# Performance work log

Measured on AMD Instinct MI355X. Metric: run time of the kernel, lower is better.

## Reference

```python
import jax, jax.numpy as jnp
import numpy as np

N = 200000          # active input voxels
GRID = 96           # voxel grid extent
_OFFS = np.array([[dx, dy, dz] for dx in (-1, 0, 1) for dy in (-1, 0, 1) for dz in (-1, 0, 1)], dtype=np.int64)  # 27 kernel offsets


def _build_kmap(cin, cout, stride):
    """Build gather/scatter kernel maps for a 3x3x3 sparse conv.
    For each offset k and each output j, find input i with coord_in[i] == coord_out[j]*stride + off[k].
    Misses scatter to sentinel row n_out (dropped) and gather row 0 (value ignored)."""
    B = int(max(cin.max(), cout.max() * stride + 1)) + 3
    key_in = (cin[:, 0].astype(np.int64) * B + cin[:, 1]) * B + cin[:, 2]
    order = np.argsort(key_in).astype(np.int32)
    sk = key_in[order]
    n_out = cout.shape[0]
    g = np.zeros((27, n_out), np.int32)
    s = np.full((27, n_out), n_out, np.int32)
    ar = np.arange(n_out, dtype=np.int32)
    co = cout.astype(np.int64)
    for k in range(27):
        q = co * stride + _OFFS[k]
        valid = (q >= 0).all(axis=1)
        qk = (q[:, 0] * B + q[:, 1]) * B + q[:, 2]
        pos = np.clip(np.searchsorted(sk, qk), 0, sk.shape[0] - 1)
        found = valid & (sk[pos] == qk)
        g[k] = np.where(found, order[pos], 0)
        s[k] = np.where(found, ar, n_out)
    return jnp.asarray(g), jnp.asarray(s)


def setup_inputs() -> dict:
    rng = np.random.RandomState(0)
    raw = rng.randint(0, GRID, size=(3 * N, 3))
    coords = np.unique(raw, axis=0)[:N]          # [N,3] unique voxel coords
    c1 = coords
    c2 = np.unique(c1 // 2, axis=0)              # stride-2 output coords
    g1, s1 = _build_kmap(c1, c1, 1)              # submanifold conv1
    g2, s2 = _build_kmap(c1, c2, 2)              # strided conv2
    g3, s3 = _build_kmap(c2, c2, 1)              # submanifold conv3
    key = jax.random.key(0)
    k1, k2, k3, k4 = jax.random.split(key, 4)
    feats = jax.random.normal(k1, (N, 4), jnp.float32)
    W1 = jax.random.normal(k2, (27, 4, 32), jnp.float32) * (1.0 / np.sqrt(27 * 4))
    W2 = jax.random.normal(k3, (27, 32, 32), jnp.float32) * (1.0 / np.sqrt(27 * 32))
    W3 = jax.random.normal(k4, (27, 32, 2), jnp.float32) * (1.0 / np.sqrt(27 * 32))
    return {"feats": feats, "W1": W1, "W2": W2, "W3": W3,
            "g1": g1, "s1": s1, "g2": g2, "s2": s2, "g3": g3, "s3": s3}


def _sparse_conv(feats, W, gidx, sidx):
    n_out = sidx.shape[1]
    c_out = W.shape[-1]
    gathered = feats[gidx]                              # [27, M, Cin] irregular gather
    contrib = jnp.einsum('kmc,kcd->kmd', gathered, W)   # per-offset GEMM
    out = jnp.zeros((n_out + 1, c_out), feats.dtype)    # +1 sentinel row for misses
    out = out.at[sidx.reshape(-1)].add(contrib.reshape(-1, c_out))  # scatter-add
    return out[:n_out]


def reference(feats, W1, W2, W3, g1, s1, g2, s2, g3, s3):
    x = _sparse_conv(feats, W1, g1, s1)
    x = _sparse_conv(x, W2, g2, s2)
    x = _sparse_conv(x, W3, g3, s3)
    return x
```

## Files before the change

### kernel.cpp

```cpp
#include <hip/hip_runtime.h>

#define CDIV(a,b) (((a)+(b)-1)/(b))

typedef __attribute__((ext_vector_type(8)))  short short8v;
typedef __attribute__((ext_vector_type(4)))  short short4v;
typedef __attribute__((ext_vector_type(16))) float f32x16;

__device__ inline unsigned short f2bf(float x) {
    unsigned u = __builtin_bit_cast(unsigned, x);
    u += 0x7fffu + ((u >> 16) & 1u);
    return (unsigned short)(u >> 16);
}

__global__ __launch_bounds__(256) void prep_feats_k(
    const float* __restrict__ feats, unsigned short* __restrict__ featsh,
    unsigned short* __restrict__ x1h, int N)
{
    int i = blockIdx.x * 256 + threadIdx.x;
    if (i < N) {
        float4 f = *reinterpret_cast<const float4*>(feats + (size_t)i * 4);
        ushort4 h; h.x = f2bf(f.x); h.y = f2bf(f.y); h.z = f2bf(f.z); h.w = f2bf(f.w);
        *reinterpret_cast<ushort4*>(featsh + (size_t)i * 4) = h;
    } else if (i == N) {
        *reinterpret_cast<ushort4*>(featsh + (size_t)N * 4) = make_ushort4(0, 0, 0, 0);
        #pragma unroll
        for (int t = 0; t < 8; ++t)
            *reinterpret_cast<ushort4*>(x1h + (size_t)N * 32 + t * 4) = make_ushort4(0, 0, 0, 0);
    }
}

__global__ __launch_bounds__(256) void prep_w_k(
    const float* __restrict__ W1, const float* __restrict__ W2,
    unsigned short* __restrict__ w2h, unsigned short* __restrict__ w1f)
{
    int i = blockIdx.x * 256 + threadIdx.x;
    if (i < 27 * 1024) {
        int k = i >> 10, c = (i >> 5) & 31, d = i & 31;
        w2h[k * 1024 + d * 32 + c] = f2bf(W2[i]);
    } else if (i < 27 * 1024 + 4096) {
        int idx = i - 27 * 1024;
        int m = idx >> 9, n = (idx >> 4) & 31, kk = idx & 15;
        int slot = 4 * m + (kk >> 2), c = kk & 3;
        float v = (slot < 27) ? W1[slot * 128 + c * 32 + n] : 0.f;
        w1f[m * 512 + n * 16 + kk] = f2bf(v);
    }
}

__global__ __launch_bounds__(256) void conv1_k(
    const unsigned short* __restrict__ featsh, const unsigned short* __restrict__ w1f,
    const int* __restrict__ g1, const int* __restrict__ s1,
    unsigned short* __restrict__ x1h, int N)
{
    int tid = threadIdx.x;
    int l = tid & 63, wv = tid >> 6;
    int r = l & 31, h = l >> 5;
    int rbase = blockIdx.x * 128 + wv * 32;
    int j = rbase + r;
    int jc = j < N ? j : N - 1;

    int gm[8][2];
    #pragma unroll
    for (int m = 0; m < 8; ++m)
        #pragma unroll
        for (int t = 0; t < 2; ++t) {
            int slot = 4 * m + 2 * h + t;
            int v = N;
            if (slot < 27 && j < N) {
                int s = s1[(size_t)slot * N + jc];
                int g = g1[(size_t)slot * N + jc];
                v = (s != N) ? g : N;
            }
            gm[m][t] = v;
        }

    f32x16 acc = {};
    const char* fb = (const char*)featsh;
    const char* wb = (const char*)w1f;
    #pragma unroll
    for (int m = 0; m < 8; ++m) {
        short4v lo = *(const short4v*)(fb + (size_t)gm[m][0] * 8);
        short4v hi = *(const short4v*)(fb + (size_t)gm[m][1] * 8);
        short8v a = __builtin_shufflevector(lo, hi, 0, 1, 2, 3, 4, 5, 6, 7);
        short8v b = *(const short8v*)(wb + (m * 512 + r * 16 + h * 8) * 2);
        acc = __builtin_amdgcn_mfma_f32_32x32x16_bf16(a, b, acc, 0, 0, 0);
    }
    #pragma unroll
    for (int reg = 0; reg < 16; ++reg) {
        int row = (reg & 3) + 8 * (reg >> 2) + 4 * h;
        int j2 = rbase + row;
        if (j2 < N) x1h[(size_t)j2 * 32 + r] = f2bf(acc[reg]);
    }
}

__global__ __launch_bounds__(256) void conv2_k(
    const unsigned short* __restrict__ x1h, const unsigned short* __restrict__ w2h,
    const int* __restrict__ g2, const int* __restrict__ s2,
    float* __restrict__ x2, int M, int N)
{
    int tid = threadIdx.x;
    int l = tid & 63, wv = tid >> 6;
    int r = l & 31, h = l >> 5;
    int rbase = blockIdx.x * 128 + wv * 32;
    int j = rbase + r;
    int jc = j < M ? j : M - 1;

    int gm[27];
    #pragma unroll
    for (int k = 0; k < 27; ++k) {
        int s = s2[(size_t)k * M + jc];
        int g = g2[(size_t)k * M + jc];
        gm[k] = (j < M && s != M) ? g : N;
    }

    f32x16 acc = {};
    const char* xb = (const char*)x1h;
    const char* wb = (const char*)w2h;
    #pragma unroll
    for (int k = 0; k < 27; ++k) {
        const char* xr = xb + (size_t)gm[k] * 64;
        short8v a0 = *(const short8v*)(xr + h * 16);
        short8v a1 = *(const short8v*)(xr + 32 + h * 16);
        short8v b0 = *(const short8v*)(wb + k * 2048 + r * 64 + h * 16);
        short8v b1 = *(const short8v*)(wb + k * 2048 + r * 64 + 32 + h * 16);
        acc = __builtin_amdgcn_mfma_f32_32x32x16_bf16(a0, b0, acc, 0, 0, 0);
        acc = __builtin_amdgcn_mfma_f32_32x32x16_bf16(a1, b1, acc, 0, 0, 0);
    }
    #pragma unroll
    for (int reg = 0; reg < 16; ++reg) {
        int row = (reg & 3) + 8 * (reg >> 2) + 4 * h;
        int j2 = rbase + row;
        if (j2 < M) x2[(size_t)j2 * 32 + r] = acc[reg];
    }
}

__global__ __launch_bounds__(256) void conv3_k(
    const float* __restrict__ x2, const float* __restrict__ W3,
    const int* __restrict__ g3, const int* __restrict__ s3,
    float* __restrict__ out, int M)
{
    __shared__ float w[27 * 64];
    int tid = threadIdx.x;
    for (int i = tid; i < 27 * 64; i += 256) w[i] = W3[i];
    __syncthreads();

    int q = tid & 3;
    int j = blockIdx.x * 64 + (tid >> 2);
    int jc = j < M ? j : M - 1;

    int gm[27];
    #pragma unroll
    for (int k = 0; k < 27; ++k) {
        int s = s3[(size_t)k * M + jc];
        int g = g3[(size_t)k * M + jc];
        gm[k] = (s != M) ? g : -1;
    }

    float a0 = 0.f, a1 = 0.f;
    #pragma unroll
    for (int k = 0; k < 27; ++k) {
        float m = gm[k] >= 0 ? 1.f : 0.f;
        int g = gm[k] >= 0 ? gm[k] : 0;
        const float* xr = x2 + (size_t)g * 32 + q * 8;
        float4 f0 = *(const float4*)(xr);
        float4 f1 = *(const float4*)(xr + 4);
        const float* wk = w + k * 64 + q * 16;
        float4 wA = *(const float4*)(wk);
        float4 wB = *(const float4*)(wk + 4);
        float4 wC = *(const float4*)(wk + 8);
        float4 wD = *(const float4*)(wk + 12);
        a0 += m * (f0.x * wA.x + f0.y * wA.z + f0.z * wB.x + f0.w * wB.z
                 + f1.x * wC.x + f1.y * wC.z + f1.z * wD.x + f1.w * wD.z);
        a1 += m * (f0.x * wA.y + f0.y * wA.w + f0.z * wB.y + f0.w * wB.w
                 + f1.x * wC.y + f1.y * wC.w + f1.z * wD.y + f1.w * wD.w);
    }
    a0 += __shfl_xor(a0, 1); a0 += __shfl_xor(a0, 2);
    a1 += __shfl_xor(a1, 1); a1 += __shfl_xor(a1, 2);
    if (q == 0 && j < M)
        *reinterpret_cast<float2*>(out + (size_t)j * 2) = make_float2(a0, a1);
}

extern "C" void kernel_launch(void* const* d_in, const int* in_sizes, int n_in,
                              void* d_out, int out_size, void* d_ws, size_t ws_size,
                              hipStream_t stream) {
    const float* feats = (const float*)d_in[0];
    const float* W1    = (const float*)d_in[1];
    const float* W2    = (const float*)d_in[2];
    const float* W3    = (const float*)d_in[3];
    const int*   g1    = (const int*)d_in[4];
    const int*   s1    = (const int*)d_in[5];
    const int*   g2    = (const int*)d_in[6];
    const int*   s2    = (const int*)d_in[7];
    const int*   g3    = (const int*)d_in[8];
    const int*   s3    = (const int*)d_in[9];

    int N = in_sizes[0] / 4;
    int M = in_sizes[6] / 27;

    char* wsb = (char*)d_ws;
    size_t off = 0;
    auto alloc = [&](size_t bytes) {
        char* p = wsb + off;
        off = (off + bytes + 255) & ~(size_t)255;
        return p;
    };
    unsigned short* x1h    = (unsigned short*)alloc((size_t)(N + 1) * 64);
    unsigned short* featsh = (unsigned short*)alloc((size_t)(N + 1) * 8);
    unsigned short* w2h    = (unsigned short*)alloc(27 * 1024 * 2);
    unsigned short* w1f    = (unsigned short*)alloc(8 * 512 * 2);
    float*          x2     = (float*)alloc((size_t)M * 128);
    float* out = (float*)d_out;

    prep_feats_k<<<CDIV(N + 1, 256), 256, 0, stream>>>(feats, featsh, x1h, N);
    prep_w_k<<<CDIV(27 * 1024 + 4096, 256), 256, 0, stream>>>(W1, W2, w2h, w1f);
    conv1_k<<<CDIV(N, 128), 256, 0, stream>>>(featsh, w1f, g1, s1, x1h, N);
    conv2_k<<<CDIV(M, 128), 256, 0, stream>>>(x1h, w2h, g2, s2, x2, M, N);
    conv3_k<<<CDIV(M, 64),  256, 0, stream>>>(x2, W3, g3, s3, out, M);
}
```

Before: 168.3 us.

## Merge prep kernels, store conv2 output as bf16, run conv3 on MFMA

Merges the two prep kernels into one launch. The weights are repacked into a lane-contiguous MFMA fragment layout so each lane does one coalesced 16-byte load. conv2 now writes bf16 activations instead of fp32, which halves the intermediate traffic and gather bytes for conv3. conv3 is rewritten to use 32x32x16 bf16 MFMA with zero-padded output columns and a sentinel zero row, replacing the scalar FMA path with LDS weights. This wastes most of the MFMA compute on padding columns and adds bf16 rounding on the conv2 output.

```diff
diff --git a/kernel.cpp b/kernel.cpp
--- a/kernel.cpp
+++ b/kernel.cpp
@@ -12,42 +12,59 @@
     return (unsigned short)(u >> 16);
 }
 
-__global__ __launch_bounds__(256) void prep_feats_k(
-    const float* __restrict__ feats, unsigned short* __restrict__ featsh,
-    unsigned short* __restrict__ x1h, int N)
+__global__ __launch_bounds__(256) void prep_k(
+    const float* __restrict__ feats, const float* __restrict__ W1,
+    const float* __restrict__ W2, const float* __restrict__ W3,
+    unsigned short* __restrict__ featsh, unsigned short* __restrict__ x1h,
+    unsigned short* __restrict__ x2h,
+    unsigned short* __restrict__ w1p, unsigned short* __restrict__ w2p,
+    unsigned short* __restrict__ w3p, int N, int M)
 {
     int i = blockIdx.x * 256 + threadIdx.x;
     if (i < N) {
         float4 f = *reinterpret_cast<const float4*>(feats + (size_t)i * 4);
         ushort4 h; h.x = f2bf(f.x); h.y = f2bf(f.y); h.z = f2bf(f.z); h.w = f2bf(f.w);
         *reinterpret_cast<ushort4*>(featsh + (size_t)i * 4) = h;
-    } else if (i == N) {
+        return;
+    }
+    if (i == N) {
         *reinterpret_cast<ushort4*>(featsh + (size_t)N * 4) = make_ushort4(0, 0, 0, 0);
         #pragma unroll
-        for (int t = 0; t < 8; ++t)
+        for (int t = 0; t < 8; ++t) {
             *reinterpret_cast<ushort4*>(x1h + (size_t)N * 32 + t * 4) = make_ushort4(0, 0, 0, 0);
-    }
-}
-
-__global__ __launch_bounds__(256) void prep_w_k(
-    const float* __restrict__ W1, const float* __restrict__ W2,
-    unsigned short* __restrict__ w2h, unsigned short* __restrict__ w1f)
-{
-    int i = blockIdx.x * 256 + threadIdx.x;
-    if (i < 27 * 1024) {
-        int k = i >> 10, c = (i >> 5) & 31, d = i & 31;
-        w2h[k * 1024 + d * 32 + c] = f2bf(W2[i]);
-    } else if (i < 27 * 1024 + 4096) {
-        int idx = i - 27 * 1024;
-        int m = idx >> 9, n = (idx >> 4) & 31, kk = idx & 15;
-        int slot = 4 * m + (kk >> 2), c = kk & 3;
-        float v = (slot < 27) ? W1[slot * 128 + c * 32 + n] : 0.f;
-        w1f[m * 512 + n * 16 + kk] = f2bf(v);
+            *reinterpret_cast<ushort4*>(x2h + (size_t)M * 32 + t * 4) = make_ushort4(0, 0, 0, 0);
+        }
+        return;
+    }
+    int j = i - (N + 1);
+    if (j < 4096) {
+        int m = j >> 9, t = j & 511, l = t >> 3, e = t & 7;
+        int h = l >> 5, r = l & 31;
+        int kk = h * 8 + e, slot = 4 * m + (kk >> 2), c = kk & 3;
+        float v = (slot < 27) ? W1[slot * 128 + c * 32 + r] : 0.f;
+        w1p[j] = f2bf(v);
+        return;
+    }
+    j -= 4096;
+    if (j < 27 * 1024) {
+        int k = j >> 10, idx = j & 1023, p = idx >> 9, t = idx & 511;
+        int l = t >> 3, e = t & 7, h = l >> 5, r = l & 31;
+        int c = p * 16 + h * 8 + e;
+        w2p[j] = f2bf(W2[k * 1024 + c * 32 + r]);
+        return;
+    }
+    j -= 27 * 1024;
+    if (j < 27 * 1024) {
+        int k = j >> 10, idx = j & 1023, p = idx >> 9, t = idx & 511;
+        int l = t >> 3, e = t & 7, h = l >> 5, r = l & 31;
+        int c = p * 16 + h * 8 + e;
+        float v = (r < 2) ? W3[k * 64 + c * 2 + r] : 0.f;
+        w3p[j] = f2bf(v);
     }
 }
 
 __global__ __launch_bounds__(256) void conv1_k(
-    const unsigned short* __restrict__ featsh, const unsigned short* __restrict__ w1f,
+    const unsigned short* __restrict__ featsh, const unsigned short* __restrict__ w1p,
     const int* __restrict__ g1, const int* __restrict__ s1,
     unsigned short* __restrict__ x1h, int N)
 {
@@ -75,13 +92,13 @@
 
     f32x16 acc = {};
     const char* fb = (const char*)featsh;
-    const char* wb = (const char*)w1f;
+    const char* wb = (const char*)w1p;
     #pragma unroll
     for (int m = 0; m < 8; ++m) {
         short4v lo = *(const short4v*)(fb + (size_t)gm[m][0] * 8);
         short4v hi = *(const short4v*)(fb + (size_t)gm[m][1] * 8);
         short8v a = __builtin_shufflevector(lo, hi, 0, 1, 2, 3, 4, 5, 6, 7);
-        short8v b = *(const short8v*)(wb + (m * 512 + r * 16 + h * 8) * 2);
+        short8v b = *(const short8v*)(wb + m * 1024 + l * 16);
         acc = __builtin_amdgcn_mfma_f32_32x32x16_bf16(a, b, acc, 0, 0, 0);
     }
     #pragma unroll
@@ -93,9 +110,9 @@
 }
 
 __global__ __launch_bounds__(256) void conv2_k(
-    const unsigned short* __restrict__ x1h, const unsigned short* __restrict__ w2h,
+    const unsigned short* __restrict__ x1h, const unsigned short* __restrict__ w2p,
     const int* __restrict__ g2, const int* __restrict__ s2,
-    float* __restrict__ x2, int M, int N)
+    unsigned short* __restrict__ x2h, int M, int N)
 {
     int tid = threadIdx.x;
     int l = tid & 63, wv = tid >> 6;
@@ -114,14 +131,14 @@
 
     f32x16 acc = {};
     const char* xb = (const char*)x1h;
-    const char* wb = (const char*)w2h;
+    const char* wb = (const char*)w2p;
     #pragma unroll
     for (int k = 0; k < 27; ++k) {
         const char* xr = xb + (size_t)gm[k] * 64;
         short8v a0 = *(const short8v*)(xr + h * 16);
         short8v a1 = *(const short8v*)(xr + 32 + h * 16);
-        short8v b0 = *(const short8v*)(wb + k * 2048 + r * 64 + h * 16);
-        short8v b1 = *(const short8v*)(wb + k * 2048 + r * 64 + 32 + h * 16);
+        short8v b0 = *(const short8v*)(wb + k * 2048 + l * 16);
+        short8v b1 = *(const short8v*)(wb + k * 2048 + 1024 + l * 16);
         acc = __builtin_amdgcn_mfma_f32_32x32x16_bf16(a0, b0, acc, 0, 0, 0);
         acc = __builtin_amdgcn_mfma_f32_32x32x16_bf16(a1, b1, acc, 0, 0, 0);
     }
@@ -129,22 +146,20 @@
     for (int reg = 0; reg < 16; ++reg) {
         int row = (reg & 3) + 8 * (reg >> 2) + 4 * h;
         int j2 = rbase + row;
-        if (j2 < M) x2[(size_t)j2 * 32 + r] = acc[reg];
+        if (j2 < M) x2h[(size_t)j2 * 32 + r] = f2bf(acc[reg]);
     }
 }
 
 __global__ __launch_bounds__(256) void conv3_k(
-    const float* __restrict__ x2, const float* __restrict__ W3,
+    const unsigned short* __restrict__ x2h, const unsigned short* __restrict__ w3p,
     const int* __restrict__ g3, const int* __restrict__ s3,
     float* __restrict__ out, int M)
 {
-    __shared__ float w[27 * 64];
     int tid = threadIdx.x;
-    for (int i = tid; i < 27 * 64; i += 256) w[i] = W3[i];
-    __syncthreads();
-
-    int q = tid & 3;
-    int j = blockIdx.x * 64 + (tid >> 2);
+    int l = tid & 63, wv = tid >> 6;
+    int r = l & 31, h = l >> 5;
+    int rbase = blockIdx.x * 128 + wv * 32;
+    int j = rbase + r;
     int jc = j < M ? j : M - 1;
 
     int gm[27];
@@ -152,31 +167,30 @@
     for (int k = 0; k < 27; ++k) {
         int s = s3[(size_t)k * M + jc];
         int g = g3[(size_t)k * M + jc];
-        gm[k] = (s != M) ? g : -1;
-    }
-
-    float a0 = 0.f, a1 = 0.f;
-    #pragma unroll
-    for (int k = 0; k < 27; ++k) {
-        float m = gm[k] >= 0 ? 1.f : 0.f;
-        int g = gm[k] >= 0 ? gm[k] : 0;
-        const float* xr = x2 + (size_t)g * 32 + q * 8;
-        float4 f0 = *(const float4*)(xr);
-        float4 f1 = *(const float4*)(xr + 4);
-        const float* wk = w + k * 64 + q * 16;
-        float4 wA = *(const float4*)(wk);
-        float4 wB = *(const float4*)(wk + 4);
-        float4 wC = *(const float4*)(wk + 8);
-        float4 wD = *(const float4*)(wk + 12);
-        a0 += m * (f0.x * wA.x + f0.y * wA.z + f0.z * wB.x + f0.w * wB.z
-                 + f1.x * wC.x + f1.y * wC.z + f1.z * wD.x + f1.w * wD.z);
-        a1 += m * (f0.x * wA.y + f0.y * wA.w + f0.z * wB.y + f0.w * wB.w
-                 + f1.x * wC.y + f1.y * wC.w + f1.z * wD.y + f1.w * wD.w);
-    }
-    a0 += __shfl_xor(a0, 1); a0 += __shfl_xor(a0, 2);
-    a1 += __shfl_xor(a1, 1); a1 += __shfl_xor(a1, 2);
-    if (q == 0 && j < M)
-        *reinterpret_cast<float2*>(out + (size_t)j * 2) = make_float2(a0, a1);
+        gm[k] = (j < M && s != M) ? g : M;
+    }
+
+    f32x16 acc = {};
+    const char* xb = (const char*)x2h;
+    const char* wb = (const char*)w3p;
+    #pragma unroll
+    for (int k = 0; k < 27; ++k) {
+        const char* xr = xb + (size_t)gm[k] * 64;
+        short8v a0 = *(const short8v*)(xr + h * 16);
+        short8v a1 = *(const short8v*)(xr + 32 + h * 16);
+        short8v b0 = *(const short8v*)(wb + k * 2048 + l * 16);
+        short8v b1 = *(const short8v*)(wb + k * 2048 + 1024 + l * 16);
+        acc = __builtin_amdgcn_mfma_f32_32x32x16_bf16(a0, b0, acc, 0, 0, 0);
+        acc = __builtin_amdgcn_mfma_f32_32x32x16_bf16(a1, b1, acc, 0, 0, 0);
+    }
+    if (r < 2) {
+        #pragma unroll
+        for (int reg = 0; reg < 16; ++reg) {
+            int row = (reg & 3) + 8 * (reg >> 2) + 4 * h;
+            int j2 = rbase + row;
+            if (j2 < M) out[(size_t)j2 * 2 + r] = acc[reg];
+        }
+    }
 }
 
 extern "C" void kernel_launch(void* const* d_in, const int* in_sizes, int n_in,
@@ -204,15 +218,17 @@
         return p;
     };
     unsigned short* x1h    = (unsigned short*)alloc((size_t)(N + 1) * 64);
+    unsigned short* x2h    = (unsigned short*)alloc((size_t)(M + 1) * 64);
     unsigned short* featsh = (unsigned short*)alloc((size_t)(N + 1) * 8);
-    unsigned short* w2h    = (unsigned short*)alloc(27 * 1024 * 2);
-    unsigned short* w1f    = (unsigned short*)alloc(8 * 512 * 2);
-    float*          x2     = (float*)alloc((size_t)M * 128);
+    unsigned short* w1p    = (unsigned short*)alloc(4096 * 2);
+    unsigned short* w2p    = (unsigned short*)alloc(27 * 1024 * 2);
+    unsigned short* w3p    = (unsigned short*)alloc(27 * 1024 * 2);
     float* out = (float*)d_out;
 
-    prep_feats_k<<<CDIV(N + 1, 256), 256, 0, stream>>>(feats, featsh, x1h, N);
-    prep_w_k<<<CDIV(27 * 1024 + 4096, 256), 256, 0, stream>>>(W1, W2, w2h, w1f);
-    conv1_k<<<CDIV(N, 128), 256, 0, stream>>>(featsh, w1f, g1, s1, x1h, N);
-    conv2_k<<<CDIV(M, 128), 256, 0, stream>>>(x1h, w2h, g2, s2, x2, M, N);
-    conv3_k<<<CDIV(M, 64),  256, 0, stream>>>(x2, W3, g3, s3, out, M);
-}
+    int prep_items = (N + 1) + 4096 + 27 * 1024 + 27 * 1024;
+    prep_k<<<CDIV(prep_items, 256), 256, 0, stream>>>(
+        feats, W1, W2, W3, featsh, x1h, x2h, w1p, w2p, w3p, N, M);
+    conv1_k<<<CDIV(N, 128), 256, 0, stream>>>(featsh, w1p, g1, s1, x1h, N);
+    conv2_k<<<CDIV(M, 128), 256, 0, stream>>>(x1h, w2p, g2, s2, x2h, M, N);
+    conv3_k<<<CDIV(M, 128), 256, 0, stream>>>(x2h, w3p, g3, s3, out, M);
+}
```

Result: no change. 169.3 us (+0.6%).
